# Kernel optimization log

Measured on AMD Instinct MI355X. Metric: run time of the kernel, lower is better.

## Reference

```python
import jax, jax.numpy as jnp
import numpy as np

V, H, L, T, B, S = 32000, 1024, 2, 64, 32, 64


def setup_inputs() -> dict:
    key = jax.random.key(0)
    ks = jax.random.split(key, 10)
    sc = 0.02
    return {
        "tokens": jax.random.randint(ks[0], (T, B), 0, V),
        "h0": jax.random.normal(ks[1], (L, B, H), jnp.float32) * sc,
        "c0": jax.random.normal(ks[2], (L, B, H), jnp.float32) * sc,
        "contexts": jax.random.normal(ks[3], (B, S, H), jnp.float32) * sc,
        "emb": jax.random.normal(ks[4], (V, H), jnp.float32) * sc,
        "W_ih": jax.random.normal(ks[5], (L, 4 * H, H), jnp.float32) * sc,
        "W_hh": jax.random.normal(ks[6], (L, 4 * H, H), jnp.float32) * sc,
        "b_ih": jnp.zeros((L, 4 * H), jnp.float32),
        "b_hh": jnp.zeros((L, 4 * H), jnp.float32),
        "W_in": jax.random.normal(ks[7], (H, H), jnp.float32) * sc,
        "b_in": jnp.zeros((H,), jnp.float32),
        "W_out": jax.random.normal(ks[8], (H, 2 * H), jnp.float32) * sc,
        "b_out": jnp.zeros((H,), jnp.float32),
    }


def _lstm_cell(x, h, c, Wih, Whh, bih, bhh):
    # PyTorch LSTMCell gate order: i, f, g, o
    gates = x @ Wih.T + bih + h @ Whh.T + bhh  # [B, 4H]
    i, f, g, o = jnp.split(gates, 4, axis=-1)
    c1 = jax.nn.sigmoid(f) * c + jax.nn.sigmoid(i) * jnp.tanh(g)
    h1 = jax.nn.sigmoid(o) * jnp.tanh(c1)
    return h1, c1


def reference(tokens, h0, c0, contexts, emb, W_ih, W_hh, b_ih, b_hh,
              W_in, b_in, W_out, b_out):
    # dropout is identity in eval mode
    embs = emb[tokens]  # [T, B, H]
    n_layers = h0.shape[0]

    def step(carry, x):
        h, c = carry
        hs, cs = [], []
        inp = x
        for l in range(n_layers):
            h1, c1 = _lstm_cell(inp, h[l], c[l], W_ih[l], W_hh[l], b_ih[l], b_hh[l])
            inp = h1
            hs.append(h1)
            cs.append(c1)
        # global (Luong general) attention
        gamma = inp @ W_in.T + b_in                      # [B, H]
        scores = jnp.einsum("bsh,bh->bs", contexts, gamma)
        w = jax.nn.softmax(scores, axis=-1)              # [B, S]
        ctx = jnp.einsum("bs,bsh->bh", w, contexts)      # [B, H]
        out = jnp.tanh(jnp.concatenate([ctx, inp], axis=-1) @ W_out.T + b_out)
        return (jnp.stack(hs), jnp.stack(cs)), (out, w)

    (hT, cT), (outputs, attns) = jax.lax.scan(step, (h0, c0), embs)
    return outputs, hT, cT  # outputs: [T, B, H]
```

## Files before the change

### kernel.cpp

```cpp
#include <hip/hip_runtime.h>
#include <hip/hip_bf16.h>

#define HDIM 1024
#define BDIM 32
#define TDIM 64
#define SDIM 64
#define NBLK 256

typedef __attribute__((ext_vector_type(8))) short short8;
typedef __attribute__((ext_vector_type(4))) short s4v;
typedef __attribute__((ext_vector_type(4))) float f32x4;
typedef __attribute__((ext_vector_type(2))) float f32x2;
typedef unsigned short ushort;
typedef unsigned int uint;

__device__ __forceinline__ float sigm(float x){ return 1.f/(1.f+expf(-x)); }
__device__ __forceinline__ ushort f2bf(float x){
  uint u = __float_as_uint(x);
  u = (u + 0x7FFF + ((u>>16)&1)) >> 16;
  return (ushort)u;
}
#define MFMA16(a,b,c) __builtin_amdgcn_mfma_f32_16x16x32_bf16((a),(b),(c),0,0,0)
#define ALD(p)     __hip_atomic_load((p), __ATOMIC_RELAXED, __HIP_MEMORY_SCOPE_AGENT)
#define AST(p,v)   __hip_atomic_store((p),(v), __ATOMIC_RELAXED, __HIP_MEMORY_SCOPE_AGENT)

__device__ __forceinline__ void load8(const char* b, s4v* r){
  asm volatile(
    "global_load_dwordx2 %0, %8, off\n\t"
    "global_load_dwordx2 %1, %8, off offset:128\n\t"
    "global_load_dwordx2 %2, %8, off offset:256\n\t"
    "global_load_dwordx2 %3, %8, off offset:384\n\t"
    "global_load_dwordx2 %4, %8, off offset:2048\n\t"
    "global_load_dwordx2 %5, %8, off offset:2176\n\t"
    "global_load_dwordx2 %6, %8, off offset:2304\n\t"
    "global_load_dwordx2 %7, %8, off offset:2432\n\t"
    : "=&v"(r[0]), "=&v"(r[1]), "=&v"(r[2]), "=&v"(r[3]),
      "=&v"(r[4]), "=&v"(r[5]), "=&v"(r[6]), "=&v"(r[7])
    : "v"(b) : "memory");
}


__global__ void init_state_kernel(const float* __restrict__ h0,
                                  ushort* __restrict__ h0h,
                                  ushort* __restrict__ h1h){
  int i = blockIdx.x*256 + threadIdx.x;
  int l = i >> 15, r = i & 32767;
  int b = r >> 10, h = r & 1023;
  ushort* dst = l ? h1h : h0h;
  dst[(h>>2)*128 + b*4 + (h&3)] = f2bf(h0[i]);
}

__global__ void bar_init_kernel(int* flags){
  for(int i=threadIdx.x; i<1024; i+=256) flags[i] = 0;
}

__global__ void fused_cast_kernel(
    const float* __restrict__ W_ih, const float* __restrict__ W_hh,
    const float* __restrict__ W_in, const float* __restrict__ W_out,
    const float* __restrict__ ctx,
    ushort* __restrict__ Wih0b, ushort* __restrict__ Whh0b,
    ushort* __restrict__ Wih1b, ushort* __restrict__ Whh1b,
    ushort* __restrict__ Winb,  ushort* __restrict__ Woutb,
    ushort* __restrict__ ctxb){
  long i = (long)blockIdx.x*256 + threadIdx.x;
  const float* src; ushort* dst; long off;
  if(i < 2097152){
    if(i < 1048576){ src=W_ih;          dst=Wih0b; off=i; }
    else           { src=W_hh;          dst=Whh0b; off=i-1048576; }
  } else if(i < 4194304){
    if(i < 3145728){ src=W_ih+4194304;  dst=Wih1b; off=i-2097152; }
    else           { src=W_hh+4194304;  dst=Whh1b; off=i-3145728; }
  } else if(i < 4456448){ src=W_in;     dst=Winb;  off=i-4194304; }
  else if(i < 4980736){   src=W_out;    dst=Woutb; off=i-4456448; }
  else {                  src=ctx;      dst=ctxb;  off=i-4980736; }
  float4 v = ((const float4*)src)[off];
  ushort4 o; o.x=f2bf(v.x); o.y=f2bf(v.y); o.z=f2bf(v.z); o.w=f2bf(v.w);
  ((ushort4*)dst)[off] = o;
}

__global__ void transpose_ctx_kernel(const float* __restrict__ ctx, ushort* __restrict__ ctxT){
  int b = blockIdx.y;
  int n = blockIdx.x*64 + (threadIdx.x & 63);
  int s0 = (threadIdx.x >> 6) * 16;
  for(int s=s0; s<s0+16; s++){
    float v = ctx[((size_t)b*SDIM + s)*HDIM + n];
    ctxT[((size_t)b*HDIM + n)*SDIM + s] = f2bf(v);
  }
}

__global__ void bias_kernel(const float* __restrict__ b_ih, const float* __restrict__ b_hh,
                            float* __restrict__ bias0, float* __restrict__ bias1){
  int i = blockIdx.x*256 + threadIdx.x;
  bias0[i] = b_ih[i] + b_hh[i];
  bias1[i] = b_ih[4096+i] + b_hh[4096+i];
}

__global__ void embed_kernel(const int* __restrict__ tokens,
                             const float* __restrict__ emb,
                             ushort* __restrict__ Xb){
  int tb = blockIdx.x;
  int tok = tokens[tb];
  const float4* src = (const float4*)(emb + (size_t)tok*HDIM);
  ushort4* dst = (ushort4*)(Xb + (size_t)tb*HDIM);
  float4 v = src[threadIdx.x];
  ushort4 o; o.x=f2bf(v.x); o.y=f2bf(v.y); o.z=f2bf(v.z); o.w=f2bf(v.w);
  dst[threadIdx.x] = o;
}

__global__ __launch_bounds__(256) void gemm_mfma_bt(
    const ushort* __restrict__ A0, const ushort* __restrict__ A1, int lda, int KSPLIT,
    const ushort* __restrict__ B, int ldb,
    const float* __restrict__ bias,
    float* __restrict__ C, int ldc, int K, int act){
  __shared__ ushort As[64][40];
  __shared__ ushort Bs[64][40];
  const int bm = blockIdx.y*64, bn = blockIdx.x*64;
  const int tid = threadIdx.x, w = tid>>6, lane = tid&63;
  const int quad = lane>>4, l16 = lane&15;
  const int mh = (w>>1)*32, nh = (w&1)*32;
  const int arow = tid>>2, aseg = (tid&3)*8;
  f32x4 acc[2][2];
  #pragma unroll
  for(int i=0;i<2;i++)
    #pragma unroll
    for(int j=0;j<2;j++) acc[i][j] = (f32x4){0.f,0.f,0.f,0.f};

  for(int k0=0;k0<K;k0+=32){
    int gk = k0 + aseg;
    const ushort* ap = (gk < KSPLIT) ? (A0 + (size_t)(bm+arow)*lda + gk)
                                     : (A1 + (size_t)(bm+arow)*lda + (gk - KSPLIT));
    *(float4*)&As[arow][aseg] = *(const float4*)ap;
    *(float4*)&Bs[arow][aseg] = *(const float4*)(B + (size_t)(bn+arow)*ldb + k0 + aseg);
    __syncthreads();
    short8 a0 = *(const short8*)&As[mh + l16][quad*8];
    short8 a1 = *(const short8*)&As[mh + 16 + l16][quad*8];
    short8 b0 = *(const short8*)&Bs[nh + l16][quad*8];
    short8 b1 = *(const short8*)&Bs[nh + 16 + l16][quad*8];
    acc[0][0] = MFMA16(a0, b0, acc[0][0]);
    acc[0][1] = MFMA16(a0, b1, acc[0][1]);
    acc[1][0] = MFMA16(a1, b0, acc[1][0]);
    acc[1][1] = MFMA16(a1, b1, acc[1][1]);
    __syncthreads();
  }
  #pragma unroll
  for(int mi=0;mi<2;mi++){
    #pragma unroll
    for(int r=0;r<4;r++){
      int row = bm + mh + mi*16 + quad*4 + r;
      #pragma unroll
      for(int ni=0;ni<2;ni++){
        int col = bn + nh + ni*16 + l16;
        float v = acc[mi][ni][r];
        if(bias) v += bias[col];
        if(act==1) v = tanhf(v);
        if(act==2) ((ushort*)C)[(size_t)row*ldc + col] = f2bf(v);
        else       C[(size_t)row*ldc + col] = v;
      }
    }
  }
}

__global__ __launch_bounds__(256,1) void lstm_skew(
    const ushort* __restrict__ Whh0b,
    const ushort* __restrict__ Wih1b,
    const ushort* __restrict__ Whh1b,
    const float*  __restrict__ G0,
    const float*  __restrict__ bias1c,
    const float*  __restrict__ c0in,
    ushort* __restrict__ h0h,
    ushort* __restrict__ h1h,
    ushort* __restrict__ inp_bf,
    float*  __restrict__ outstate,
    int* __restrict__ flags){
  extern __shared__ char smem[];
  ushort (*W0s)[1032]   = (ushort(*)[1032])smem;
  ushort (*W1s)[2056]   = (ushort(*)[2056])(smem + 33024);
  typedef float gredT[4][32][17];
  gredT* gred0 = (gredT*)(smem + 98816);
  gredT* gred1 = (gredT*)(smem + 116224);
  float (*cloc0)[4]      = (float(*)[4])(smem + 133632);
  float (*cloc1)[4]      = (float(*)[4])(smem + 134144);

  const int tid = threadIdx.x, w = tid>>6, lane = tid&63;
  const int quad = lane>>4, l16 = lane&15;
  const int blk = blockIdx.x;
  const int j0 = blk*4;

  {
    int r = tid>>4, seg = tid&15;
    int wr = (r>>2)*1024 + j0 + (r&3);
    const ushort* s0 = Whh0b + (size_t)wr*1024 + seg*64;
    const ushort* s1 = Wih1b + (size_t)wr*1024 + seg*64;
    const ushort* s2 = Whh1b + (size_t)wr*1024 + seg*64;
    #pragma unroll
    for(int u=0; u<64; u+=8){
      *(short8*)&W0s[r][seg*64+u]       = *(const short8*)(s0+u);
      *(short8*)&W1s[r][seg*64+u]       = *(const short8*)(s1+u);
      *(short8*)&W1s[r][1024+seg*64+u]  = *(const short8*)(s2+u);
    }
  }
  if(tid < 128){
    int b = tid>>2, jj = tid&3;
    cloc0[b][jj] = c0in[b*1024 + j0 + jj];
    cloc1[b][jj] = c0in[32768 + b*1024 + j0 + jj];
  }
  float2 pbI={0,0}, pbF={0,0}, pbG={0,0}, pbO={0,0};
  if(tid >= 64 && tid < 128){
    const float* br = bias1c + j0 + ((tid-64)&1)*2;
    pbI = *(const float2*)(br);
    pbF = *(const float2*)(br+1024);
    pbG = *(const float2*)(br+2048);
    pbO = *(const float2*)(br+3072);
  }
  __syncthreads();

  for(int p=0; p<=TDIM+1; p++){
    const int par = p&1;
    const bool doL0 = (p < TDIM);
    const bool doL1 = (p >= 2);
    const ushort* h0p    = h0h + (size_t)p*32768;
    ushort*       h0n    = h0h + (size_t)(p+1)*32768;
    const ushort* h0prev = h0h + (size_t)(p>=1?p-1:0)*32768;
    const ushort* h1m    = h1h + (size_t)(p>=2?p-2:0)*32768;
    ushort*       h1c    = h1h + (size_t)(p>=1?p-1:0)*32768;

    f32x4 accA0 = {0,0,0,0}, accA1 = {0,0,0,0};

    f32x2 pgI={0,0}, pgF={0,0}, pgG={0,0}, pgO={0,0};
    if(doL0 && tid < 64){
      const float* g0r = G0 + (size_t)(p*32+(tid>>1))*4096 + j0 + (tid&1)*2;
      asm volatile(
        "global_load_dwordx2 %0, %4, off\n\t"
        "global_load_dwordx2 %1, %5, off\n\t"
        "global_load_dwordx2 %2, %6, off\n\t"
        "global_load_dwordx2 %3, %7, off"
        : "=&v"(pgI), "=&v"(pgF), "=&v"(pgG), "=&v"(pgO)
        : "v"(g0r), "v"(g0r+1024), "v"(g0r+2048), "v"(g0r+3072)
        : "memory");
    }
    {
      s4v ra[32];
      if(doL1){
        const char* ba = (const char*)h0prev + w*16384 + quad*512 + l16*8;
        load8(ba,       ra);
        load8(ba+4096,  ra+8);
        load8(ba+8192,  ra+16);
        load8(ba+12288, ra+24);
      }
      asm volatile("s_waitcnt vmcnt(0)" ::: "memory");
      __builtin_amdgcn_sched_barrier(0);
      if(doL1){
        #pragma unroll
        for(int kc=0;kc<8;kc++){
          short8 af0 = __builtin_shufflevector(ra[kc*4+0], ra[kc*4+2], 0,1,2,3,4,5,6,7);
          short8 af1 = __builtin_shufflevector(ra[kc*4+1], ra[kc*4+3], 0,1,2,3,4,5,6,7);
          short8 bfrag = *(const short8*)&W1s[l16][w*256 + kc*32 + quad*8];
          accA0 = MFMA16(af0, bfrag, accA0);
          accA1 = MFMA16(af1, bfrag, accA1);
        }
      }
    }

    if(p >= 1){
      const int target = p;
      if(blk==0 && tid<64){
        while(true){
          int mn = 0x7fffffff;
          #pragma unroll
          for(int q=0;q<8;q++){ int v = ALD(&flags[tid + q*64]); mn = min(mn, v); }
          if(__all(mn >= target)) break;
          __builtin_amdgcn_s_sleep(1);
        }
        if(tid < 16) AST(&flags[512 + tid*32], target);
      }
      while(ALD(&flags[512 + (blk>>4)*32]) < target) __builtin_amdgcn_s_sleep(1);
    }

    {
      s4v rb[32], rc[32];
      if(doL0){
        const char* bb = (const char*)h0p + w*16384 + quad*512 + l16*8;
        load8(bb,       rb);
        load8(bb+4096,  rb+8);
        load8(bb+8192,  rb+16);
        load8(bb+12288, rb+24);
      }
      if(doL1){
        const char* bc = (const char*)h1m + w*16384 + quad*512 + l16*8;
        load8(bc,       rc);
        load8(bc+4096,  rc+8);
        load8(bc+8192,  rc+16);
        load8(bc+12288, rc+24);
      }
      if(doL0){
        if(doL1) asm volatile("s_waitcnt vmcnt(32)" ::: "memory");
        else     asm volatile("s_waitcnt vmcnt(0)"  ::: "memory");
        __builtin_amdgcn_sched_barrier(0);
        f32x4 acc0 = {0,0,0,0}, acc1 = {0,0,0,0};
        #pragma unroll
        for(int kc=0;kc<8;kc++){
          short8 af0 = __builtin_shufflevector(rb[kc*4+0], rb[kc*4+2], 0,1,2,3,4,5,6,7);
          short8 af1 = __builtin_shufflevector(rb[kc*4+1], rb[kc*4+3], 0,1,2,3,4,5,6,7);
          short8 bfrag = *(const short8*)&W0s[l16][w*256 + kc*32 + quad*8];
          acc0 = MFMA16(af0, bfrag, acc0);
          acc1 = MFMA16(af1, bfrag, acc1);
        }
        #pragma unroll
        for(int r=0;r<4;r++){
          gred0[par][w][quad*4+r][l16]    = acc0[r];
          gred0[par][w][16+quad*4+r][l16] = acc1[r];
        }
      }
      if(doL1){
        asm volatile("s_waitcnt vmcnt(0)" ::: "memory");
        __builtin_amdgcn_sched_barrier(0);
        #pragma unroll
        for(int kc=0;kc<8;kc++){
          short8 af0 = __builtin_shufflevector(rc[kc*4+0], rc[kc*4+2], 0,1,2,3,4,5,6,7);
          short8 af1 = __builtin_shufflevector(rc[kc*4+1], rc[kc*4+3], 0,1,2,3,4,5,6,7);
          short8 bfrag = *(const short8*)&W1s[l16][1024 + w*256 + kc*32 + quad*8];
          accA0 = MFMA16(af0, bfrag, accA0);
          accA1 = MFMA16(af1, bfrag, accA1);
        }
        #pragma unroll
        for(int r=0;r<4;r++){
          gred1[par][w][quad*4+r][l16]    = accA0[r];
          gred1[par][w][16+quad*4+r][l16] = accA1[r];
        }
      }
    }
    __syncthreads();

    if(doL0 && tid < 64){
      int b = tid>>1, j2 = (tid&1)*2;
      ushort hv[2];
      #pragma unroll
      for(int u=0;u<2;u++){
        int jj = j2+u;
        float gi = u ? pgI.y : pgI.x;
        float gf = u ? pgF.y : pgF.x;
        float gg = u ? pgG.y : pgG.x;
        float go = u ? pgO.y : pgO.x;
        #pragma unroll
        for(int ww=0;ww<4;ww++){
          gi += gred0[par][ww][b][jj];    gf += gred0[par][ww][b][4+jj];
          gg += gred0[par][ww][b][8+jj];  go += gred0[par][ww][b][12+jj];
        }
        float c = cloc0[b][jj];
        float c1 = sigm(gf)*c + sigm(gi)*tanhf(gg);
        float h1 = sigm(go)*tanhf(c1);
        cloc0[b][jj] = c1;
        hv[u] = f2bf(h1);
        if(p==TDIM-1){
          outstate[b*1024 + j0 + jj] = h1;
          outstate[65536 + b*1024 + j0 + jj] = c1;
        }
      }
      uint pk = (uint)hv[0] | ((uint)hv[1] << 16);
      AST((uint*)(h0n + blk*128 + b*4 + j2), pk);
    }
    if(doL1 && tid >= 64 && tid < 128){
      int ct = tid-64;
      int b = ct>>1, j2 = (ct&1)*2;
      ushort hv[2];
      #pragma unroll
      for(int u=0;u<2;u++){
        int jj = j2+u;
        float gi = u ? pbI.y : pbI.x;
        float gf = u ? pbF.y : pbF.x;
        float gg = u ? pbG.y : pbG.x;
        float go = u ? pbO.y : pbO.x;
        #pragma unroll
        for(int ww=0;ww<4;ww++){
          gi += gred1[par][ww][b][jj];    gf += gred1[par][ww][b][4+jj];
          gg += gred1[par][ww][b][8+jj];  go += gred1[par][ww][b][12+jj];
        }
        float c = cloc1[b][jj];
        float c1 = sigm(gf)*c + sigm(gi)*tanhf(gg);
        float h1 = sigm(go)*tanhf(c1);
        cloc1[b][jj] = c1;
        hv[u] = f2bf(h1);
        inp_bf[(size_t)((p-2)*32+b)*1024 + j0 + jj] = hv[u];
        if(p==TDIM+1){
          outstate[32768 + b*1024 + j0 + jj] = h1;
          outstate[98304 + b*1024 + j0 + jj] = c1;
        }
      }
      uint pk = (uint)hv[0] | ((uint)hv[1] << 16);
      AST((uint*)(h1c + blk*128 + b*4 + j2), pk);
    }
    if(p == TDIM+1) break;

    if(tid < 128){
      asm volatile("s_waitcnt vmcnt(0)" ::: "memory");
      if((tid&63)==0) AST(&flags[blk*2 + w], p+1);
    }
  }
}

__global__ __launch_bounds__(256) void attn_mfma(
    const ushort* __restrict__ gamma_bf,
    const ushort* __restrict__ ctxb,
    const ushort* __restrict__ ctxT,
    ushort* __restrict__ ctx_out){
  const int b = blockIdx.y, t0 = blockIdx.x*16;
  const int tid = threadIdx.x, w = tid>>6, lane = tid&63;
  const int quad = lane>>4, l16 = lane&15;
  __shared__ float S[16][68];
  __shared__ ushort Pb[16][72];
  {
    f32x4 acc = {0,0,0,0};
    const ushort* arow = gamma_bf + ((size_t)(t0+l16)*32 + b)*1024;
    const ushort* brow = ctxb + ((size_t)b*SDIM + w*16 + l16)*1024;
    #pragma unroll 8
    for(int kc=0;kc<32;kc++){
      short8 af = *(const short8*)(arow + kc*32 + quad*8);
      short8 bf = *(const short8*)(brow + kc*32 + quad*8);
      acc = MFMA16(af, bf, acc);
    }
    #pragma unroll
    for(int r=0;r<4;r++) S[quad*4+r][w*16+l16] = acc[r];
  }
  __syncthreads();
  if(tid < 16){
    float mx = -1e30f;
    for(int s=0;s<SDIM;s++) mx = fmaxf(mx, S[tid][s]);
    float sum = 0.f;
    for(int s=0;s<SDIM;s++) sum += expf(S[tid][s]-mx);
    float inv = 1.f/sum;
    for(int s=0;s<SDIM;s++) Pb[tid][s] = f2bf(expf(S[tid][s]-mx)*inv);
  }
  __syncthreads();
  const ushort* bbase = ctxT + ((size_t)b*HDIM + w*256)*SDIM;
  for(int nt=0; nt<16; nt++){
    f32x4 acc = {0,0,0,0};
    #pragma unroll
    for(int kc=0;kc<2;kc++){
      short8 af = *(const short8*)&Pb[l16][kc*32 + quad*8];
      short8 bf = *(const short8*)(bbase + (size_t)(nt*16+l16)*SDIM + kc*32 + quad*8);
      acc = MFMA16(af, bf, acc);
    }
    int n = w*256 + nt*16 + l16;
    #pragma unroll
    for(int r=0;r<4;r++){
      int t = t0 + quad*4 + r;
      ctx_out[((size_t)t*32 + b)*1024 + n] = f2bf(acc[r]);
    }
  }
}

extern "C" void kernel_launch(void* const* d_in, const int* in_sizes, int n_in,
                              void* d_out, int out_size, void* d_ws, size_t ws_size,
                              hipStream_t stream){
  const int*   tokens   = (const int*)  d_in[0];
  const float* h0       = (const float*)d_in[1];
  const float* c0       = (const float*)d_in[2];
  const float* contexts = (const float*)d_in[3];
  const float* emb      = (const float*)d_in[4];
  const float* W_ih     = (const float*)d_in[5];
  const float* W_hh     = (const float*)d_in[6];
  const float* b_ih     = (const float*)d_in[7];
  const float* b_hh     = (const float*)d_in[8];
  const float* W_in     = (const float*)d_in[9];
  const float* b_in     = (const float*)d_in[10];
  const float* W_out    = (const float*)d_in[11];
  const float* b_out    = (const float*)d_in[12];

  float* out = (float*)d_out;
  const int TB = TDIM*BDIM;

  char* wp = (char*)d_ws;
  float* G0      = (float*)wp;  wp += (size_t)TB*4*HDIM*4;
  float* bias0c  = (float*)wp;  wp += 4096*4;
  float* bias1c  = (float*)wp;  wp += 4096*4;
  int*   flags   = (int*)wp;    wp += 4096;
  ushort* X_bf   = (ushort*)wp; wp += (size_t)TB*HDIM*2;
  ushort* Wih0b  = (ushort*)wp; wp += (size_t)4*HDIM*HDIM*2;
  ushort* Whh0b  = (ushort*)wp; wp += (size_t)4*HDIM*HDIM*2;
  ushort* Wih1b  = (ushort*)wp; wp += (size_t)4*HDIM*HDIM*2;
  ushort* Whh1b  = (ushort*)wp; wp += (size_t)4*HDIM*HDIM*2;
  ushort* Winb   = (ushort*)wp; wp += (size_t)HDIM*HDIM*2;
  ushort* Woutb  = (ushort*)wp; wp += (size_t)HDIM*2*HDIM*2;
  ushort* inp_bf = (ushort*)wp; wp += (size_t)TB*HDIM*2;
  ushort* h0hist = (ushort*)wp; wp += (size_t)(TDIM+2)*BDIM*HDIM*2;
  ushort* h1hist = (ushort*)wp; wp += (size_t)(TDIM+1)*BDIM*HDIM*2;
  ushort* ctxb_bf= (ushort*)wp; wp += (size_t)BDIM*SDIM*HDIM*2;
  ushort* ctxT_bf= (ushort*)wp; wp += (size_t)BDIM*SDIM*HDIM*2;
  ushort* gammaB = (ushort*)G0;
  ushort* ctx_bf = X_bf;

  init_state_kernel<<<256,256,0,stream>>>(h0, h0hist, h1hist);
  bar_init_kernel<<<1,256,0,stream>>>(flags);
  fused_cast_kernel<<<21504,256,0,stream>>>(
      W_ih, W_hh, W_in, W_out, contexts,
      Wih0b, Whh0b, Wih1b, Whh1b, Winb, Woutb, ctxb_bf);
  transpose_ctx_kernel<<<dim3(16,32),256,0,stream>>>(contexts, ctxT_bf);
  bias_kernel<<<16,256,0,stream>>>(b_ih, b_hh, bias0c, bias1c);
  embed_kernel<<<TB,256,0,stream>>>(tokens, emb, X_bf);

  gemm_mfma_bt<<<dim3(4*HDIM/64, TB/64),256,0,stream>>>(
      X_bf, X_bf, HDIM, HDIM, Wih0b, HDIM, bias0c, G0, 4*HDIM, HDIM, 0);

  lstm_skew<<<NBLK,256,134656,stream>>>(
      Whh0b, Wih1b, Whh1b, G0, bias1c, c0,
      h0hist, h1hist, inp_bf, out + (size_t)TB*HDIM, flags);

  gemm_mfma_bt<<<dim3(HDIM/64, TB/64),256,0,stream>>>(
      inp_bf, inp_bf, HDIM, HDIM, Winb, HDIM, b_in, (float*)gammaB, HDIM, HDIM, 2);

  attn_mfma<<<dim3(4,32),256,0,stream>>>(gammaB, ctxb_bf, ctxT_bf, ctx_bf);

  gemm_mfma_bt<<<dim3(HDIM/64, TB/64),256,0,stream>>>(
      ctx_bf, inp_bf, HDIM, HDIM, Woutb, 2*HDIM, b_out, out, HDIM, 2*HDIM, 1);
}
```

Before: 820.1 us.

## Enlarge GEMM tiles to 128x128 with register-prefetched K slices

Replaces the 64x64-tile bf16 MFMA GEMM with a 128x128-tile version where each wave computes a 64x64 sub-tile (4x4 MFMA accumulators). The next K slice is loaded from global memory into registers while the current slice is consumed from LDS. This aims to raise arithmetic intensity and hide global load latency. The trade-off is fewer blocks: the N=1024 GEMMs launch only 128 blocks, fewer than the GPU has CUs, and register pressure is higher.

```diff
diff --git a/kernel.cpp b/kernel.cpp
--- a/kernel.cpp
+++ b/kernel.cpp
@@ -107,49 +107,67 @@
   dst[threadIdx.x] = o;
 }
 
-__global__ __launch_bounds__(256) void gemm_mfma_bt(
+__global__ __launch_bounds__(256) void gemm128(
     const ushort* __restrict__ A0, const ushort* __restrict__ A1, int lda, int KSPLIT,
     const ushort* __restrict__ B, int ldb,
     const float* __restrict__ bias,
     float* __restrict__ C, int ldc, int K, int act){
-  __shared__ ushort As[64][40];
-  __shared__ ushort Bs[64][40];
-  const int bm = blockIdx.y*64, bn = blockIdx.x*64;
+  __shared__ ushort As[128][40];
+  __shared__ ushort Bs[128][40];
+  const int bm = blockIdx.y*128, bn = blockIdx.x*128;
   const int tid = threadIdx.x, w = tid>>6, lane = tid&63;
   const int quad = lane>>4, l16 = lane&15;
-  const int mh = (w>>1)*32, nh = (w&1)*32;
-  const int arow = tid>>2, aseg = (tid&3)*8;
-  f32x4 acc[2][2];
+  const int wr = (w>>1)*64, wc = (w&1)*64;
+  const int srow = tid>>2, sseg = (tid&3)*8;
+  f32x4 acc[4][4];
   #pragma unroll
-  for(int i=0;i<2;i++)
-    #pragma unroll
-    for(int j=0;j<2;j++) acc[i][j] = (f32x4){0.f,0.f,0.f,0.f};
-
+  for(int i=0;i<4;i++)
+    #pragma unroll
+    for(int j=0;j<4;j++) acc[i][j] = (f32x4){0.f,0.f,0.f,0.f};
+
+  float4 ra0, ra1, rb0, rb1;
+  {
+    int gk = sseg;
+    const ushort* ap = (gk < KSPLIT) ? (A0 + (size_t)(bm+srow)*lda + gk)
+                                     : (A1 + (size_t)(bm+srow)*lda + (gk-KSPLIT));
+    ra0 = *(const float4*)ap;  ra1 = *(const float4*)(ap + (size_t)64*lda);
+    const ushort* bp = B + (size_t)(bn+srow)*ldb + gk;
+    rb0 = *(const float4*)bp;  rb1 = *(const float4*)(bp + (size_t)64*ldb);
+  }
   for(int k0=0;k0<K;k0+=32){
-    int gk = k0 + aseg;
-    const ushort* ap = (gk < KSPLIT) ? (A0 + (size_t)(bm+arow)*lda + gk)
-                                     : (A1 + (size_t)(bm+arow)*lda + (gk - KSPLIT));
-    *(float4*)&As[arow][aseg] = *(const float4*)ap;
-    *(float4*)&Bs[arow][aseg] = *(const float4*)(B + (size_t)(bn+arow)*ldb + k0 + aseg);
     __syncthreads();
-    short8 a0 = *(const short8*)&As[mh + l16][quad*8];
-    short8 a1 = *(const short8*)&As[mh + 16 + l16][quad*8];
-    short8 b0 = *(const short8*)&Bs[nh + l16][quad*8];
-    short8 b1 = *(const short8*)&Bs[nh + 16 + l16][quad*8];
-    acc[0][0] = MFMA16(a0, b0, acc[0][0]);
-    acc[0][1] = MFMA16(a0, b1, acc[0][1]);
-    acc[1][0] = MFMA16(a1, b0, acc[1][0]);
-    acc[1][1] = MFMA16(a1, b1, acc[1][1]);
+    *(float4*)&As[srow][sseg]    = ra0;
+    *(float4*)&As[srow+64][sseg] = ra1;
+    *(float4*)&Bs[srow][sseg]    = rb0;
+    *(float4*)&Bs[srow+64][sseg] = rb1;
     __syncthreads();
+    if(k0+32 < K){
+      int gk = k0 + 32 + sseg;
+      const ushort* ap = (gk < KSPLIT) ? (A0 + (size_t)(bm+srow)*lda + gk)
+                                       : (A1 + (size_t)(bm+srow)*lda + (gk-KSPLIT));
+      ra0 = *(const float4*)ap;  ra1 = *(const float4*)(ap + (size_t)64*lda);
+      const ushort* bp = B + (size_t)(bn+srow)*ldb + k0 + 32 + sseg;
+      rb0 = *(const float4*)bp;  rb1 = *(const float4*)(bp + (size_t)64*ldb);
+    }
+    short8 af[4], bf[4];
+    #pragma unroll
+    for(int mi=0;mi<4;mi++) af[mi] = *(const short8*)&As[wr+mi*16+l16][quad*8];
+    #pragma unroll
+    for(int ni=0;ni<4;ni++) bf[ni] = *(const short8*)&Bs[wc+ni*16+l16][quad*8];
+    #pragma unroll
+    for(int mi=0;mi<4;mi++)
+      #pragma unroll
+      for(int ni=0;ni<4;ni++)
+        acc[mi][ni] = MFMA16(af[mi], bf[ni], acc[mi][ni]);
   }
   #pragma unroll
-  for(int mi=0;mi<2;mi++){
+  for(int mi=0;mi<4;mi++){
     #pragma unroll
     for(int r=0;r<4;r++){
-      int row = bm + mh + mi*16 + quad*4 + r;
+      int row = bm + wr + mi*16 + quad*4 + r;
       #pragma unroll
-      for(int ni=0;ni<2;ni++){
-        int col = bn + nh + ni*16 + l16;
+      for(int ni=0;ni<4;ni++){
+        int col = bn + wc + ni*16 + l16;
         float v = acc[mi][ni][r];
         if(bias) v += bias[col];
         if(act==1) v = tanhf(v);
@@ -498,18 +516,18 @@
   bias_kernel<<<16,256,0,stream>>>(b_ih, b_hh, bias0c, bias1c);
   embed_kernel<<<TB,256,0,stream>>>(tokens, emb, X_bf);
 
-  gemm_mfma_bt<<<dim3(4*HDIM/64, TB/64),256,0,stream>>>(
+  gemm128<<<dim3(4*HDIM/128, TB/128),256,0,stream>>>(
       X_bf, X_bf, HDIM, HDIM, Wih0b, HDIM, bias0c, G0, 4*HDIM, HDIM, 0);
 
   lstm_skew<<<NBLK,256,134656,stream>>>(
       Whh0b, Wih1b, Whh1b, G0, bias1c, c0,
       h0hist, h1hist, inp_bf, out + (size_t)TB*HDIM, flags);
 
-  gemm_mfma_bt<<<dim3(HDIM/64, TB/64),256,0,stream>>>(
+  gemm128<<<dim3(HDIM/128, TB/128),256,0,stream>>>(
       inp_bf, inp_bf, HDIM, HDIM, Winb, HDIM, b_in, (float*)gammaB, HDIM, HDIM, 2);
 
   attn_mfma<<<dim3(4,32),256,0,stream>>>(gammaB, ctxb_bf, ctxT_bf, ctx_bf);
 
-  gemm_mfma_bt<<<dim3(HDIM/64, TB/64),256,0,stream>>>(
+  gemm128<<<dim3(HDIM/128, TB/128),256,0,stream>>>(
       ctx_bf, inp_bf, HDIM, HDIM, Woutb, 2*HDIM, b_out, out, HDIM, 2*HDIM, 1);
 }
```

Result: faster. 780.9 us (-4.8%).
